# Performance work log

Measured on AMD Instinct MI355X. Metric: run time of the kernel, lower is better.

The kernel has to match this reference:

```python
import jax, jax.numpy as jnp
import numpy as np

B, S, DIM, N, D = 1, 2688, 1536, 12, 128
C = D // 2  # 64 complex pairs per head
EPS = 1e-06


def rms_norm(x, g, eps=EPS):
    # x: [B, S, DIM] -- norm over full model dim, as in WanRMSNorm
    xf = x.astype(jnp.float32)
    return (xf * jax.lax.rsqrt(jnp.mean(xf * xf, axis=-1, keepdims=True) + eps)) * g


def rope_apply(x, f, h, w, freqs_c):
    # x: [B, S, N, D]; freqs_c: complex64 [1024, C]; f*h*w == S (full-seq case)
    s1 = C - 2 * (C // 3)  # 22 (temporal)
    s2 = C // 3            # 21 (height), 21 (width)
    ff = freqs_c[:f, :s1]
    fh = freqs_c[:h, s1:s1 + s2]
    fw = freqs_c[:w, s1 + s2:]
    fi = jnp.concatenate([
        jnp.broadcast_to(ff[:, None, None, :], (f, h, w, s1)),
        jnp.broadcast_to(fh[None, :, None, :], (f, h, w, s2)),
        jnp.broadcast_to(fw[None, None, :, :], (f, h, w, s2)),
    ], axis=-1).reshape(f * h * w, 1, C)  # [S, 1, C]
    xr = x.astype(jnp.float32).reshape(B, S, N, C, 2)
    xc = jax.lax.complex(xr[..., 0], xr[..., 1])          # [B, S, N, C]
    out = xc * fi[None]                                    # broadcast over B, N
    return jnp.stack([out.real, out.imag], axis=-1).reshape(B, S, N, D)


def setup_inputs() -> dict:
    key = jax.random.key(0)
    ks = jax.random.split(key, 12)
    w_scale = 0.02
    # deterministic rope angles (faithful structure: exp(i*theta) per axis slice)
    pos = np.arange(1024, dtype=np.float32)
    inv = 1.0 / (10000.0 ** (np.arange(C, dtype=np.float32) / C))
    ang = pos[:, None] * inv[None, :]
    return {
        "x": jax.random.normal(ks[0], (B, S, DIM), jnp.float32),
        "seq_lens": jnp.full((B,), S, dtype=jnp.int32),
        "grid_sizes": jnp.array([[6, 16, 28]], dtype=jnp.int32),
        "freqs_cos": jnp.asarray(np.cos(ang), jnp.float32),
        "freqs_sin": jnp.asarray(np.sin(ang), jnp.float32),
        "Wq": jax.random.normal(ks[1], (DIM, DIM), jnp.float32) * w_scale,
        "bq": jnp.zeros((DIM,), jnp.float32),
        "Wk": jax.random.normal(ks[2], (DIM, DIM), jnp.float32) * w_scale,
        "bk": jnp.zeros((DIM,), jnp.float32),
        "Wv": jax.random.normal(ks[3], (DIM, DIM), jnp.float32) * w_scale,
        "bv": jnp.zeros((DIM,), jnp.float32),
        "Wo": jax.random.normal(ks[4], (DIM, DIM), jnp.float32) * w_scale,
        "bo": jnp.zeros((DIM,), jnp.float32),
        "gq": jnp.ones((DIM,), jnp.float32),
        "gk": jnp.ones((DIM,), jnp.float32),
    }


def reference(x, seq_lens, grid_sizes, freqs_cos, freqs_sin,
              Wq, bq, Wk, bk, Wv, bv, Wo, bo, gq, gk):
    f, h, w = (int(grid_sizes[0, 0]), int(grid_sizes[0, 1]), int(grid_sizes[0, 2]))
    freqs_c = jax.lax.complex(freqs_cos, freqs_sin)  # [1024, C]

    q = rms_norm(x @ Wq.T + bq, gq).reshape(B, S, N, D)
    k = rms_norm(x @ Wk.T + bk, gk).reshape(B, S, N, D)
    v = (x @ Wv.T + bv).reshape(B, S, N, D)

    q = rope_apply(q, f, h, w, freqs_c)
    k = rope_apply(k, f, h, w, freqs_c)

    # SDPA with key-length masking (k_lens)
    scale = 1.0 / jnp.sqrt(jnp.float32(D))
    scores = jnp.einsum("bqnd,bknd->bnqk", q, k) * scale  # [B, N, S, S]
    kmask = jnp.arange(S)[None, :] < seq_lens[:, None]     # [B, S]
    scores = jnp.where(kmask[:, None, None, :], scores, -jnp.inf)
    attn = jax.nn.softmax(scores, axis=-1)
    out = jnp.einsum("bnqk,bknd->bqnd", attn, v).reshape(B, S, DIM)
    return out @ Wo.T + bo
```

## Files before the change

### kernel.cpp

```cpp
#include <hip/hip_runtime.h>
#include <hip/hip_bf16.h>
#include <stdint.h>

#define S_LEN 2688
#define DIM   1536
#define NH    12
#define HD    128
#define QKV_N 4608

typedef __attribute__((ext_vector_type(8))) short bf16x8;
typedef __attribute__((ext_vector_type(4))) float f32x4;

__device__ inline ushort f2bf(float f) {
    uint32_t u = __float_as_uint(f);
    uint32_t r = (u + 0x7fffu + ((u >> 16) & 1u)) >> 16;
    return (ushort)r;
}
__device__ inline float bf2f(uint u) { return __uint_as_float(u << 16); }
__device__ inline float fexp2(float x) {
    float r;
    asm("v_exp_f32 %0, %1" : "=v"(r) : "v"(x));
    return r;
}
__device__ inline uint cvtpk(float lo, float hi) {
    uint r;
    asm("v_cvt_pk_bf16_f32 %0, %1, %2" : "=v"(r) : "v"(lo), "v"(hi));
    return r;
}

#define GLOAD16(gp, lp) __builtin_amdgcn_global_load_lds( \
    (__attribute__((address_space(1))) const void*)(gp),  \
    (__attribute__((address_space(3))) void*)(lp), 16, 0, 0)

__global__ __launch_bounds__(256) void convert_all(
    const float* __restrict__ x,
    const float* __restrict__ wq, const float* __restrict__ wk,
    const float* __restrict__ wv, const float* __restrict__ wo,
    ushort* __restrict__ xb, ushort* __restrict__ wb)
{
    const size_t NX4 = (size_t)S_LEN * DIM / 4;
    const size_t NW4 = (size_t)DIM * DIM / 4;
    size_t i = (size_t)blockIdx.x * 256 + threadIdx.x;
    const float* src; ushort* dst;
    if (i < NX4)            { src = x;  dst = xb; }
    else if (i < NX4+1*NW4) { src = wq; dst = wb;                        i -= NX4; }
    else if (i < NX4+2*NW4) { src = wk; dst = wb + 1*(size_t)DIM*DIM;    i -= NX4+1*NW4; }
    else if (i < NX4+3*NW4) { src = wv; dst = wb + 2*(size_t)DIM*DIM;    i -= NX4+2*NW4; }
    else if (i < NX4+4*NW4) { src = wo; dst = wb + 3*(size_t)DIM*DIM;    i -= NX4+3*NW4; }
    else return;
    float4 v = reinterpret_cast<const float4*>(src)[i];
    ushort4 o = { f2bf(v.x), f2bf(v.y), f2bf(v.z), f2bf(v.w) };
    reinterpret_cast<ushort4*>(dst)[i] = o;
}

__global__ __launch_bounds__(256) void gemm_qkv(
    const ushort* __restrict__ A, const ushort* __restrict__ B,
    const float* __restrict__ bq, const float* __restrict__ bk,
    const float* __restrict__ bv,
    ushort* __restrict__ qkb, ushort* __restrict__ v_t, int K)
{
    __shared__ ushort At[128 * 64];
    __shared__ ushort Bt[128 * 64];
    const int tid  = threadIdx.x;
    const int wave = tid >> 6, lane = tid & 63;
    const int m0 = blockIdx.x * 128, n0 = blockIdx.y * 128;
    const int wr = wave >> 1, wc = wave & 1;
    const int r = lane & 15, g = lane >> 4;
    const int srow = wave * 8 + (lane >> 3);
    const int scol = (lane & 7) * 8;

    f32x4 acc[4][4] = {};

    for (int k0 = 0; k0 < K; k0 += 64) {
        const ushort* Ag = A + (size_t)m0 * K + k0;
        const ushort* Bg = B + (size_t)n0 * K + k0;
#pragma unroll
        for (int t = 0; t < 4; ++t) {
            GLOAD16(Ag + (size_t)(t*32 + srow) * K + scol, &At[t*2048 + wave*512]);
            GLOAD16(Bg + (size_t)(t*32 + srow) * K + scol, &Bt[t*2048 + wave*512]);
        }
        asm volatile("s_waitcnt vmcnt(0)" ::: "memory");
        __syncthreads();
#pragma unroll
        for (int kk = 0; kk < 2; ++kk) {
            bf16x8 af[4], bfr[4];
#pragma unroll
            for (int i = 0; i < 4; ++i)
                af[i] = *reinterpret_cast<const bf16x8*>(
                    &At[(wr*64 + i*16 + r) * 64 + kk*32 + g*8]);
#pragma unroll
            for (int i = 0; i < 4; ++i)
                bfr[i] = *reinterpret_cast<const bf16x8*>(
                    &Bt[(wc*64 + i*16 + r) * 64 + kk*32 + g*8]);
#pragma unroll
            for (int mi = 0; mi < 4; ++mi)
#pragma unroll
                for (int ni = 0; ni < 4; ++ni)
                    acc[mi][ni] = __builtin_amdgcn_mfma_f32_16x16x32_bf16(
                        af[mi], bfr[ni], acc[mi][ni], 0, 0, 0);
        }
        __syncthreads();
    }

    if (n0 < 2*DIM) {
#pragma unroll
        for (int ni = 0; ni < 4; ++ni) {
            int col = n0 + wc*64 + ni*16 + r;
            float bias = (col < DIM) ? bq[col] : bk[col - DIM];
#pragma unroll
            for (int mi = 0; mi < 4; ++mi) {
                int row = m0 + wr*64 + mi*16 + g*4;
#pragma unroll
                for (int j = 0; j < 4; ++j)
                    qkb[(size_t)(row + j) * (2*DIM) + col] =
                        f2bf(acc[mi][ni][j] + bias);
            }
        }
    } else {
#pragma unroll
        for (int ni = 0; ni < 4; ++ni) {
            int d = n0 - 2*DIM + wc*64 + ni*16 + r;
            float bias = bv[d];
#pragma unroll
            for (int mi = 0; mi < 4; ++mi) {
                int row = m0 + wr*64 + mi*16 + g*4;
                uint2 pkt;
                pkt.x = cvtpk(acc[mi][ni][0] + bias, acc[mi][ni][1] + bias);
                pkt.y = cvtpk(acc[mi][ni][2] + bias, acc[mi][ni][3] + bias);
                *reinterpret_cast<uint2*>(&v_t[(size_t)d * S_LEN + row]) = pkt;
            }
        }
    }
}

__global__ __launch_bounds__(256) void gemm_bt2(
    const ushort* __restrict__ A, const ushort* __restrict__ B,
    const float* __restrict__ b0,
    float* __restrict__ C, int M, int N, int K)
{
    __shared__ ushort At[128 * 64];
    __shared__ ushort Bt[64 * 64];
    const int tid  = threadIdx.x;
    const int wave = tid >> 6, lane = tid & 63;
    const int m0 = blockIdx.x * 128, n0 = blockIdx.y * 64;
    const int wr = wave >> 1, wc = wave & 1;
    const int r = lane & 15, g = lane >> 4;
    const int srow = wave * 8 + (lane >> 3);
    const int scol = (lane & 7) * 8;
    const int brow[2] = { (0*256+tid)>>3, (1*256+tid)>>3 };
    const int bcol = (tid & 7) * 8;

    f32x4 acc[4][2] = {};

    for (int k0 = 0; k0 < K; k0 += 64) {
        const ushort* Ag = A + (size_t)m0 * K + k0;
        const ushort* Bg = B + (size_t)n0 * K + k0;
#pragma unroll
        for (int t = 0; t < 4; ++t)
            GLOAD16(Ag + (size_t)(t*32 + srow) * K + scol, &At[t*2048 + wave*512]);
#pragma unroll
        for (int t = 0; t < 2; ++t)
            GLOAD16(Bg + (size_t)brow[t] * K + bcol, &Bt[(t*256 + wave*64) * 8]);
        asm volatile("s_waitcnt vmcnt(0)" ::: "memory");
        __syncthreads();
#pragma unroll
        for (int kk = 0; kk < 2; ++kk) {
            bf16x8 af[4], bfr[2];
#pragma unroll
            for (int i = 0; i < 4; ++i)
                af[i] = *reinterpret_cast<const bf16x8*>(
                    &At[(wr*64 + i*16 + r) * 64 + kk*32 + g*8]);
#pragma unroll
            for (int i = 0; i < 2; ++i)
                bfr[i] = *reinterpret_cast<const bf16x8*>(
                    &Bt[(wc*32 + i*16 + r) * 64 + kk*32 + g*8]);
#pragma unroll
            for (int mi = 0; mi < 4; ++mi)
#pragma unroll
                for (int ni = 0; ni < 2; ++ni)
                    acc[mi][ni] = __builtin_amdgcn_mfma_f32_16x16x32_bf16(
                        af[mi], bfr[ni], acc[mi][ni], 0, 0, 0);
        }
        __syncthreads();
    }

#pragma unroll
    for (int ni = 0; ni < 2; ++ni) {
        int col = n0 + wc*32 + ni*16 + r;
        float bias = b0[col];
#pragma unroll
        for (int mi = 0; mi < 4; ++mi) {
            int row = m0 + wr*64 + mi*16 + g*4;
#pragma unroll
            for (int j = 0; j < 4; ++j)
                C[(size_t)(row + j) * N + col] = acc[mi][ni][j] + bias;
        }
    }
}

__global__ __launch_bounds__(256) void normrope(
    const ushort* __restrict__ qkb, const int* __restrict__ gsz,
    const float* __restrict__ gq, const float* __restrict__ gk,
    const float* __restrict__ fcos, const float* __restrict__ fsin,
    ushort* __restrict__ q_r, ushort* __restrict__ k_r)
{
    const int s   = blockIdx.x;
    const int tid = threadIdx.x;
    const int wave = tid >> 6, lane = tid & 63;
    const uint* qrow = reinterpret_cast<const uint*>(qkb + (size_t)s * (2*DIM));
    const uint* krow = qrow + DIM/2;

    float2 qv[3], kv[3];
    float sq = 0.f, sk = 0.f;
#pragma unroll
    for (int i = 0; i < 3; ++i) {
        int p = tid + i*256;
        uint uq = qrow[p], uk = krow[p];
        qv[i].x = bf2f(uq & 0xffffu); qv[i].y = bf2f(uq >> 16);
        kv[i].x = bf2f(uk & 0xffffu); kv[i].y = bf2f(uk >> 16);
        sq += qv[i].x*qv[i].x + qv[i].y*qv[i].y;
        sk += kv[i].x*kv[i].x + kv[i].y*kv[i].y;
    }
#pragma unroll
    for (int off = 1; off < 64; off <<= 1) {
        sq += __shfl_xor(sq, off);
        sk += __shfl_xor(sk, off);
    }
    __shared__ float red[4][2];
    if (lane == 0) { red[wave][0] = sq; red[wave][1] = sk; }
    __syncthreads();
    sq = red[0][0] + red[1][0] + red[2][0] + red[3][0];
    sk = red[0][1] + red[1][1] + red[2][1] + red[3][1];
    const float rmsq = rsqrtf(sq * (1.f/DIM) + 1e-6f);
    const float rmsk = rsqrtf(sk * (1.f/DIM) + 1e-6f);

    const int hh = gsz[1], ww = gsz[2];
    const int fidx = s / (hh*ww), rem = s % (hh*ww);
    const int hidx = rem / ww,  widx = rem % ww;
    const float qscale = rmsq * (0.08838834764831845f * 1.4426950408889634f);

#pragma unroll
    for (int i = 0; i < 3; ++i) {
        int p = tid + i*256;
        int c = p & 63, head = p >> 6;
        int coord = (c < 22) ? fidx : (c < 43) ? hidx : widx;
        float cv = fcos[coord*64 + c], sv = fsin[coord*64 + c];
        float2 gqv = reinterpret_cast<const float2*>(gq)[p];
        float2 gkv = reinterpret_cast<const float2*>(gk)[p];
        float a = qv[i].x * qscale * gqv.x, b = qv[i].y * qscale * gqv.y;
        uint qo = cvtpk(a*cv - b*sv, a*sv + b*cv);
        a = kv[i].x * rmsk * gkv.x; b = kv[i].y * rmsk * gkv.y;
        uint ko = cvtpk(a*cv - b*sv, a*sv + b*cv);
        size_t off = (((size_t)head * S_LEN + s) * HD + 2*c) >> 1;
        reinterpret_cast<uint*>(q_r)[off] = qo;
        reinterpret_cast<uint*>(k_r)[off] = ko;
    }
}

__global__ __launch_bounds__(256) void attn_fwd(
    const ushort* __restrict__ q_r, const ushort* __restrict__ k_r,
    const ushort* __restrict__ v_t, const int* __restrict__ seq_lens,
    ushort* __restrict__ attn_out)
{
    __shared__ ushort Kl[2][64 * 128];
    __shared__ ushort Vl[2][128 * 64];
    __shared__ ushort Pl[4][16 * 72];
    const int tid  = threadIdx.x;
    const int wave = tid >> 6, lane = tid & 63;
    const int n  = blockIdx.y;
    const int q0 = blockIdx.x * 64 + wave * 16;
    const int seq = seq_lens[0];
    const int r = lane & 15, g = lane >> 4;
    const int swz = r & 7;
    const ushort* Qh = q_r + (size_t)n * S_LEN * HD;
    const ushort* Kh = k_r + (size_t)n * S_LEN * HD;
    const ushort* Vh = v_t + (size_t)n * HD * S_LEN;

    const int kj_row[4] = { (0*256+tid)>>4, (1*256+tid)>>4, (2*256+tid)>>4, (3*256+tid)>>4 };
    const int kj_w  = tid & 15;
    const int vj_d[4]  = { (0*256+tid)>>3, (1*256+tid)>>3, (2*256+tid)>>3, (3*256+tid)>>3 };
    const int vj_w  = tid & 7;

    bf16x8 qf[4];
#pragma unroll
    for (int c = 0; c < 4; ++c)
        qf[c] = *reinterpret_cast<const bf16x8*>(Qh + (size_t)(q0 + r) * HD + c*32 + g*8);

    f32x4 oacc[8] = {};
    float mrun = -1e30f, lrun = 0.f;

    const int nt = (seq + 63) >> 6;

#define STAGE(buf, kbase)                                                     \
    do {                                                                      \
        _Pragma("unroll")                                                     \
        for (int t = 0; t < 4; ++t) {                                         \
            int row = kj_row[t];                                              \
            GLOAD16(Kh + (size_t)((kbase) + row) * HD + ((kj_w ^ (row & 7)) * 8), \
                    &Kl[buf][(t*256 + wave*64) * 8]);                         \
        }                                                                     \
        _Pragma("unroll")                                                     \
        for (int t = 0; t < 4; ++t) {                                         \
            int d = vj_d[t];                                                  \
            GLOAD16(Vh + (size_t)d * S_LEN + (kbase) + ((vj_w ^ (d & 7)) * 8), \
                    &Vl[buf][(t*256 + wave*64) * 8]);                         \
        }                                                                     \
    } while (0)

    STAGE(0, 0);
    asm volatile("s_waitcnt vmcnt(0)" ::: "memory");
    __syncthreads();

    int cur = 0;
    for (int kt = 0; kt < nt; ++kt) {
        const int k0 = kt * 64;
        if (kt + 1 < nt) STAGE(cur ^ 1, k0 + 64);

        f32x4 sf[4];
#pragma unroll
        for (int kb = 0; kb < 4; ++kb) {
            f32x4 s = {0.f, 0.f, 0.f, 0.f};
            const ushort* kl = &Kl[cur][(kb*16 + r) * 128];
#pragma unroll
            for (int c = 0; c < 4; ++c)
                s = __builtin_amdgcn_mfma_f32_16x16x32_bf16(
                    *reinterpret_cast<const bf16x8*>(kl + ((4*c + g) ^ swz) * 8),
                    qf[c], s, 0, 0, 0);
            sf[kb] = s;
        }
        if (k0 + 64 > seq) {
#pragma unroll
            for (int kb = 0; kb < 4; ++kb)
#pragma unroll
                for (int j = 0; j < 4; ++j)
                    if (k0 + kb*16 + g*4 + j >= seq) sf[kb][j] = -1e30f;
        }
        float pm = fmaxf(fmaxf(fmaxf(sf[0][0], sf[0][1]), fmaxf(sf[0][2], sf[0][3])),
                         fmaxf(fmaxf(sf[1][0], sf[1][1]), fmaxf(sf[1][2], sf[1][3])));
        pm = fmaxf(pm, fmaxf(fmaxf(fmaxf(sf[2][0], sf[2][1]), fmaxf(sf[2][2], sf[2][3])),
                             fmaxf(fmaxf(sf[3][0], sf[3][1]), fmaxf(sf[3][2], sf[3][3]))));
        pm = fmaxf(pm, __shfl_xor(pm, 16));
        pm = fmaxf(pm, __shfl_xor(pm, 32));
        if (!__all(pm - mrun <= 8.f)) {
            float mn = fmaxf(mrun, pm);
            float scl = fexp2(mrun - mn);
            mrun = mn;
            lrun *= scl;
#pragma unroll
            for (int f = 0; f < 8; ++f)
#pragma unroll
                for (int j = 0; j < 4; ++j) oacc[f][j] *= scl;
        }
        float ps = 0.f;
#pragma unroll
        for (int kb = 0; kb < 4; ++kb) {
            float e0 = fexp2(sf[kb][0] - mrun), e1 = fexp2(sf[kb][1] - mrun);
            float e2 = fexp2(sf[kb][2] - mrun), e3 = fexp2(sf[kb][3] - mrun);
            sf[kb][0] = e0; sf[kb][1] = e1; sf[kb][2] = e2; sf[kb][3] = e3;
            ps += (e0 + e1) + (e2 + e3);
        }
        ps += __shfl_xor(ps, 16);
        ps += __shfl_xor(ps, 32);
        lrun += ps;
#pragma unroll
        for (int kb = 0; kb < 4; ++kb) {
            uint2 pkt;
            pkt.x = cvtpk(sf[kb][0], sf[kb][1]);
            pkt.y = cvtpk(sf[kb][2], sf[kb][3]);
            *reinterpret_cast<uint2*>(&Pl[wave][r*72 + kb*16 + g*4]) = pkt;
        }
        bf16x8 pf[2];
        pf[0] = *reinterpret_cast<const bf16x8*>(&Pl[wave][r*72 + g*8]);
        pf[1] = *reinterpret_cast<const bf16x8*>(&Pl[wave][r*72 + 32 + g*8]);
#pragma unroll
        for (int db = 0; db < 8; ++db) {
            const ushort* vl = &Vl[cur][(db*16 + r) * 64];
#pragma unroll
            for (int kb2 = 0; kb2 < 2; ++kb2)
                oacc[db] = __builtin_amdgcn_mfma_f32_16x16x32_bf16(
                    *reinterpret_cast<const bf16x8*>(vl + ((kb2*4 + g) ^ swz) * 8),
                    pf[kb2], oacc[db], 0, 0, 0);
        }

        if (kt + 1 < nt) {
            asm volatile("s_waitcnt vmcnt(0)" ::: "memory");
            __syncthreads();
            cur ^= 1;
        }
    }
#undef STAGE

    const float inv = (lrun > 0.f) ? 1.f / lrun : 0.f;
#pragma unroll
    for (int db = 0; db < 8; ++db) {
        uint2 pkt;
        pkt.x = cvtpk(oacc[db][0]*inv, oacc[db][1]*inv);
        pkt.y = cvtpk(oacc[db][2]*inv, oacc[db][3]*inv);
        *reinterpret_cast<uint2*>(
            &attn_out[(size_t)(q0 + r) * DIM + n*HD + db*16 + g*4]) = pkt;
    }
}

extern "C" void kernel_launch(void* const* d_in, const int* in_sizes, int n_in,
                              void* d_out, int out_size, void* d_ws, size_t ws_size,
                              hipStream_t stream)
{
    const float* x    = (const float*)d_in[0];
    const int*   seqL = (const int*)  d_in[1];
    const int*   gsz  = (const int*)  d_in[2];
    const float* fcos = (const float*)d_in[3];
    const float* fsin = (const float*)d_in[4];
    const float* Wq   = (const float*)d_in[5];
    const float* bq   = (const float*)d_in[6];
    const float* Wk   = (const float*)d_in[7];
    const float* bk   = (const float*)d_in[8];
    const float* Wv   = (const float*)d_in[9];
    const float* bv   = (const float*)d_in[10];
    const float* Wo   = (const float*)d_in[11];
    const float* bo   = (const float*)d_in[12];
    const float* gq   = (const float*)d_in[13];
    const float* gk   = (const float*)d_in[14];
    float* out = (float*)d_out;

    char* ws = (char*)d_ws;
    ushort* xb  = (ushort*)ws;
    ushort* wb  = xb  + (size_t)S_LEN * DIM;
    ushort* qkb = wb  + 4*(size_t)DIM*DIM;
    ushort* v_t = qkb + (size_t)S_LEN * 2*DIM;
    ushort* q_r = v_t + (size_t)DIM * S_LEN;
    ushort* k_r = q_r + (size_t)S_LEN * DIM;
    ushort* ao  = k_r + (size_t)S_LEN * DIM;

    convert_all<<<13248, 256, 0, stream>>>(x, Wq, Wk, Wv, Wo, xb, wb);
    gemm_qkv<<<dim3(21, 36), 256, 0, stream>>>(xb, wb, bq, bk, bv,
                                               qkb, v_t, DIM);
    normrope<<<S_LEN, 256, 0, stream>>>(qkb, gsz, gq, gk, fcos, fsin, q_r, k_r);
    attn_fwd<<<dim3(42, 12), 256, 0, stream>>>(q_r, k_r, v_t, seqL, ao);
    gemm_bt2<<<dim3(21, 24), 256, 0, stream>>>(ao, wb + 3*(size_t)DIM*DIM,
                                               bo, out, S_LEN, DIM, DIM);
}
```

Baseline: 219.2 us.

## Load V fragments directly from global into registers and add MFMA priority hints

Drops the shared-memory staging of the V tile. Each lane now loads its V operand fragments straight from global memory into registers at the start of every key tile, and the PV MFMAs consume them directly. It also wraps the QK and PV MFMA blocks in s_setprio to raise wave priority during matrix work. This cuts LDS footprint and LDS traffic, which may allow more blocks per CU, but it adds per-lane global loads with less coalescing and register pressure from 16 bf16x8 fragments. Those loads are also not double-buffered, so their latency may be exposed.

```diff
diff --git a/kernel.cpp b/kernel.cpp
--- a/kernel.cpp
+++ b/kernel.cpp
@@ -263,7 +263,6 @@
     ushort* __restrict__ attn_out)
 {
     __shared__ ushort Kl[2][64 * 128];
-    __shared__ ushort Vl[2][128 * 64];
     __shared__ ushort Pl[4][16 * 72];
     const int tid  = threadIdx.x;
     const int wave = tid >> 6, lane = tid & 63;
@@ -278,8 +277,7 @@
 
     const int kj_row[4] = { (0*256+tid)>>4, (1*256+tid)>>4, (2*256+tid)>>4, (3*256+tid)>>4 };
     const int kj_w  = tid & 15;
-    const int vj_d[4]  = { (0*256+tid)>>3, (1*256+tid)>>3, (2*256+tid)>>3, (3*256+tid)>>3 };
-    const int vj_w  = tid & 7;
+    const ushort* Vbase = Vh + (size_t)r * S_LEN + g*8;
 
     bf16x8 qf[4];
 #pragma unroll
@@ -291,7 +289,7 @@
 
     const int nt = (seq + 63) >> 6;
 
-#define STAGE(buf, kbase)                                                     \
+#define STAGE_K(buf, kbase)                                                   \
     do {                                                                      \
         _Pragma("unroll")                                                     \
         for (int t = 0; t < 4; ++t) {                                         \
@@ -299,24 +297,27 @@
             GLOAD16(Kh + (size_t)((kbase) + row) * HD + ((kj_w ^ (row & 7)) * 8), \
                     &Kl[buf][(t*256 + wave*64) * 8]);                         \
         }                                                                     \
-        _Pragma("unroll")                                                     \
-        for (int t = 0; t < 4; ++t) {                                         \
-            int d = vj_d[t];                                                  \
-            GLOAD16(Vh + (size_t)d * S_LEN + (kbase) + ((vj_w ^ (d & 7)) * 8), \
-                    &Vl[buf][(t*256 + wave*64) * 8]);                         \
-        }                                                                     \
     } while (0)
 
-    STAGE(0, 0);
+    STAGE_K(0, 0);
     asm volatile("s_waitcnt vmcnt(0)" ::: "memory");
     __syncthreads();
 
     int cur = 0;
     for (int kt = 0; kt < nt; ++kt) {
         const int k0 = kt * 64;
-        if (kt + 1 < nt) STAGE(cur ^ 1, k0 + 64);
+        if (kt + 1 < nt) STAGE_K(cur ^ 1, k0 + 64);
+
+        bf16x8 vf[8][2];
+#pragma unroll
+        for (int db = 0; db < 8; ++db)
+#pragma unroll
+            for (int kb2 = 0; kb2 < 2; ++kb2)
+                vf[db][kb2] = *reinterpret_cast<const bf16x8*>(
+                    Vbase + (size_t)(db*16) * S_LEN + k0 + kb2*32);
 
         f32x4 sf[4];
+        __builtin_amdgcn_s_setprio(1);
 #pragma unroll
         for (int kb = 0; kb < 4; ++kb) {
             f32x4 s = {0.f, 0.f, 0.f, 0.f};
@@ -328,6 +329,7 @@
                     qf[c], s, 0, 0, 0);
             sf[kb] = s;
         }
+        __builtin_amdgcn_s_setprio(0);
         if (k0 + 64 > seq) {
 #pragma unroll
             for (int kb = 0; kb < 4; ++kb)
@@ -372,15 +374,14 @@
         bf16x8 pf[2];
         pf[0] = *reinterpret_cast<const bf16x8*>(&Pl[wave][r*72 + g*8]);
         pf[1] = *reinterpret_cast<const bf16x8*>(&Pl[wave][r*72 + 32 + g*8]);
-#pragma unroll
-        for (int db = 0; db < 8; ++db) {
-            const ushort* vl = &Vl[cur][(db*16 + r) * 64];
+        __builtin_amdgcn_s_setprio(1);
+#pragma unroll
+        for (int db = 0; db < 8; ++db)
 #pragma unroll
             for (int kb2 = 0; kb2 < 2; ++kb2)
                 oacc[db] = __builtin_amdgcn_mfma_f32_16x16x32_bf16(
-                    *reinterpret_cast<const bf16x8*>(vl + ((kb2*4 + g) ^ swz) * 8),
-                    pf[kb2], oacc[db], 0, 0, 0);
-        }
+                    vf[db][kb2], pf[kb2], oacc[db], 0, 0, 0);
+        __builtin_amdgcn_s_setprio(0);
 
         if (kt + 1 < nt) {
             asm volatile("s_waitcnt vmcnt(0)" ::: "memory");
@@ -388,7 +389,7 @@
             cur ^= 1;
         }
     }
-#undef STAGE
+#undef STAGE_K
 
     const float inv = (lrun > 0.f) ? 1.f / lrun : 0.f;
 #pragma unroll
```

New measurement: 314.0 us. +43.3%, slower.
